# Optimization experiments

Hardware: AMD Instinct MI355X
Metric: run time of the kernel (lower is better)

Reference implementation:

```python
import jax, jax.numpy as jnp
import numpy as np

N_NODES = 20000
N_EDGES = 320000
IN_FEATS = 256
H_FEATS = 256


def setup_inputs() -> dict:
    key = jax.random.key(0)
    ks = jax.random.split(key, 8)
    s = 1.0 / np.sqrt(IN_FEATS)
    return {
        "features": jax.random.normal(ks[0], (N_NODES, IN_FEATS), jnp.float32),
        "src": jax.random.randint(ks[1], (N_EDGES,), 0, N_NODES, jnp.int32),
        "dst": jax.random.randint(ks[2], (N_EDGES,), 0, N_NODES, jnp.int32),
        "W_self1": jax.random.normal(ks[3], (IN_FEATS, H_FEATS), jnp.float32) * s,
        "W_neigh1": jax.random.normal(ks[4], (IN_FEATS, H_FEATS), jnp.float32) * s,
        "b1": jnp.zeros((H_FEATS,), jnp.float32),
        "W_self2": jax.random.normal(ks[5], (H_FEATS, H_FEATS), jnp.float32) * s,
        "W_neigh2": jax.random.normal(ks[6], (H_FEATS, H_FEATS), jnp.float32) * s,
        "b2": jnp.zeros((H_FEATS,), jnp.float32),
    }


def _sage_conv(h, src, dst, W_self, W_neigh, b, n_nodes):
    # mean aggregation of src features onto dst nodes (DGL SAGEConv 'mean')
    msg_sum = jax.ops.segment_sum(h[src], dst, num_segments=n_nodes)  # [N, d]
    deg = jax.ops.segment_sum(jnp.ones_like(dst, dtype=h.dtype), dst,
                              num_segments=n_nodes)  # [N]
    h_neigh = msg_sum / jnp.maximum(deg, 1.0)[:, None]  # isolated nodes -> 0
    return h @ W_self + h_neigh @ W_neigh + b


def reference(features, src, dst, W_self1, W_neigh1, b1, W_self2, W_neigh2, b2):
    n = features.shape[0]
    h = _sage_conv(features, src, dst, W_self1, W_neigh1, b1, n)
    h = jax.nn.relu(h)
    h = _sage_conv(h, src, dst, W_self2, W_neigh2, b2, n)
    # DotPredictor: per-edge dot product of src/dst embeddings
    score = jnp.sum(h[src] * h[dst], axis=1)  # [E]
    return score
```

## Files before the change

kernel.cpp:

```cpp
#include <hip/hip_runtime.h>
#include <hip/hip_bf16.h>
#include <stdint.h>

typedef __bf16 bf16_t;
typedef __bf16 bf16x8 __attribute__((ext_vector_type(8)));
typedef __bf16 bf16x4 __attribute__((ext_vector_type(4)));
typedef float f32x4 __attribute__((ext_vector_type(4)));

#define NFEAT 256
#define KDIM  512
#define BM 64
#define BN 128
#define BK 64

__device__ __forceinline__ void gload_lds16(const void* g, void* l) {
  __builtin_amdgcn_global_load_lds(
      (const __attribute__((address_space(1))) unsigned int*)g,
      (__attribute__((address_space(3))) unsigned int*)l, 16, 0, 0);
}

__device__ int g_b1, g_b2, g_b3, g_done;
__device__ int g_part[128];

__device__ __forceinline__ void grid_bar(int* ctr, int nb) {
  __syncthreads();
  if (threadIdx.x == 0) {
    __threadfence();
    atomicAdd(ctr, 1);
    while (atomicAdd(ctr, 0) < nb) { }
  }
  __syncthreads();
}

__global__ __launch_bounds__(256) void k_graph(
    const int* __restrict__ src, const int* __restrict__ dst,
    int* __restrict__ deg, int* __restrict__ offsets, int* __restrict__ cursor,
    float* __restrict__ inv_deg, int* __restrict__ csr_src, int2* __restrict__ epack,
    int nE, int n, int nb) {
  const int b   = blockIdx.x;
  const int tid = threadIdx.x;
  const int gt  = b * 256 + tid;
  const int G   = nb * 256;

  for (int e = gt; e < nE; e += G) atomicAdd(&deg[dst[e]], 1);
  grid_bar(&g_b1, nb);

  __shared__ int s[256], p[256];
  const int i = b * 256 + tid;
  const int d = (i < n) ? atomicAdd(&deg[i], 0) : 0;
  s[tid] = d;
  __syncthreads();
  for (int off = 1; off < 256; off <<= 1) {
    int v = (tid >= off) ? s[tid - off] : 0;
    __syncthreads();
    s[tid] += v;
    __syncthreads();
  }
  if (tid == 255) atomicExch(&g_part[b], s[255]);
  grid_bar(&g_b2, nb);

  int pv = 0;
  if (tid < b) pv = atomicAdd(&g_part[tid], 0);
  p[tid] = pv;
  __syncthreads();
  for (int off = 128; off; off >>= 1) {
    if (tid < off) p[tid] += p[tid + off];
    __syncthreads();
  }
  const int block_excl = p[0];
  if (i < n) {
    int excl = block_excl + s[tid] - d;
    offsets[i] = excl;
    atomicExch(&cursor[i], excl);
    inv_deg[i] = 1.0f / (float)(d > 1 ? d : 1);
  }
  grid_bar(&g_b3, nb);

  for (int e = gt; e < nE; e += G) {
    int dd = dst[e];
    int ss = src[e];
    int pos = atomicAdd(&cursor[dd], 1);
    csr_src[pos] = ss;
    epack[pos] = make_int2((dd << 16) | ss, e);
  }

  __syncthreads();
  if (tid == 0) {
    int old = atomicAdd(&g_done, 1);
    if (old == nb - 1) {
      atomicExch(&g_b1, 0);
      atomicExch(&g_b2, 0);
      atomicExch(&g_b3, 0);
      atomicExch(&g_done, 0);
    }
  }
}

__global__ void k_prep(const float* __restrict__ F,
                       const float* __restrict__ Ws1, const float* __restrict__ Wn1,
                       const float* __restrict__ Ws2, const float* __restrict__ Wn2,
                       bf16_t* __restrict__ WT1, bf16_t* __restrict__ WT2,
                       bf16_t* __restrict__ X,
                       int* __restrict__ deg, int nNodes, int mpad) {
  int t = blockIdx.x * blockDim.x + threadIdx.x;
  if (t < mpad) deg[t] = 0;
  if (t < 2 * NFEAT * KDIM) {
    int layer = t >> 17;
    int r = t & (NFEAT * KDIM - 1);
    int n = r >> 9;
    int k = r & 511;
    const float* Ws = layer ? Ws2 : Ws1;
    const float* Wn = layer ? Wn2 : Wn1;
    float v = (k < NFEAT) ? Ws[k * NFEAT + n] : Wn[(k - NFEAT) * NFEAT + n];
    (layer ? WT2 : WT1)[r] = (bf16_t)v;
  }
  int n = t >> 6;
  int c = (t & 63) * 4;
  if (n < mpad) {
    float4 v = make_float4(0.f, 0.f, 0.f, 0.f);
    if (n < nNodes) v = *(const float4*)&F[(size_t)n * NFEAT + c];
    bf16x4 o;
    o[0] = (bf16_t)v.x; o[1] = (bf16_t)v.y; o[2] = (bf16_t)v.z; o[3] = (bf16_t)v.w;
    *(bf16x4*)&X[(size_t)n * KDIM + c] = o;
  }
}

__global__ __launch_bounds__(256) void k_agg(const bf16_t* __restrict__ Hin,
                                             bf16_t* __restrict__ Hout,
                                             const int* __restrict__ csr_src,
                                             const int* __restrict__ offsets,
                                             const int* __restrict__ deg,
                                             const float* __restrict__ inv_deg,
                                             int instride, int outstride) {
  const int n   = blockIdx.x * 8 + (threadIdx.x >> 5);
  const int l32 = threadIdx.x & 31;
  const int beg = offsets[n];
  const int cnt = deg[n];
  const size_t colo = (size_t)l32 * 8;

  float acc[8] = {0.f, 0.f, 0.f, 0.f, 0.f, 0.f, 0.f, 0.f};

  int s[4];
  #pragma unroll
  for (int q = 0; q < 4; ++q) s[q] = (q < cnt) ? csr_src[beg + q] : -1;

  for (int i = 0; i < cnt; i += 4) {
    bf16x8 v[4];
    bool h[4];
    #pragma unroll
    for (int q = 0; q < 4; ++q) {
      h[q] = (s[q] >= 0);
      if (h[q]) v[q] = *(const bf16x8*)&Hin[(size_t)s[q] * instride + colo];
    }
    #pragma unroll
    for (int q = 0; q < 4; ++q) {
      int j = i + 4 + q;
      s[q] = (j < cnt) ? csr_src[beg + j] : -1;
    }
    #pragma unroll
    for (int q = 0; q < 4; ++q) {
      if (h[q]) {
        #pragma unroll
        for (int e = 0; e < 8; ++e) acc[e] += (float)v[q][e];
      }
    }
  }

  float w = inv_deg[n];
  bf16x8 o;
  #pragma unroll
  for (int e = 0; e < 8; ++e) o[e] = (bf16_t)(acc[e] * w);
  *(bf16x8*)&Hout[(size_t)n * outstride + NFEAT + colo] = o;
}

__global__ __launch_bounds__(256, 3) void k_gemm(const bf16_t* __restrict__ A,
                                                 const bf16_t* __restrict__ BT,
                                                 const float* __restrict__ bias,
                                                 bf16_t* __restrict__ Cout,
                                                 int ostride, int relu) {
  __shared__ __align__(16) bf16_t As[2][BM * BK];
  __shared__ __align__(16) bf16_t Bs[2][BN * BK];
  const int tid  = threadIdx.x;
  const int lane = tid & 63;
  const int wave = tid >> 6;
  const int wr = wave >> 1, wc = wave & 1;
  const int m0 = blockIdx.x * BM;
  const int n0 = blockIdx.y * BN;
  const int l15 = lane & 15;
  const int lk8 = (lane >> 4) * 8;

  f32x4 acc[2][4] = {};

  auto stage = [&](int buf, int kt) {
    const int k0 = kt * BK;
    #pragma unroll
    for (int i = 0; i < 2; ++i) {
      int idx = i * 256 + tid;
      int row = idx >> 3;
      int c8  = (idx & 7) * 8;
      gload_lds16(A + (size_t)(m0 + row) * KDIM + k0 + c8,
                  (char*)&As[buf][0] + (i * 256 + wave * 64) * 16);
    }
    #pragma unroll
    for (int i = 0; i < 4; ++i) {
      int idx = i * 256 + tid;
      int row = idx >> 3;
      int c8  = (idx & 7) * 8;
      gload_lds16(BT + (size_t)(n0 + row) * KDIM + k0 + c8,
                  (char*)&Bs[buf][0] + (i * 256 + wave * 64) * 16);
    }
  };

  auto compute = [&](int buf) {
    #pragma unroll
    for (int kk = 0; kk < 2; ++kk) {
      bf16x8 af[2], bfr[4];
      #pragma unroll
      for (int m = 0; m < 2; ++m) {
        int row = wr * 32 + m * 16 + l15;
        af[m] = *(const bf16x8*)&As[buf][row * BK + kk * 32 + lk8];
      }
      #pragma unroll
      for (int n = 0; n < 4; ++n) {
        int col = wc * 64 + n * 16 + l15;
        bfr[n] = *(const bf16x8*)&Bs[buf][col * BK + kk * 32 + lk8];
      }
      #pragma unroll
      for (int m = 0; m < 2; ++m)
        #pragma unroll
        for (int n = 0; n < 4; ++n)
          acc[m][n] = __builtin_amdgcn_mfma_f32_16x16x32_bf16(af[m], bfr[n], acc[m][n], 0, 0, 0);
    }
  };

  stage(0, 0);
  __syncthreads();
  const int nt = KDIM / BK;
  int cur = 0;
  for (int t = 0; t < nt; ++t) {
    if (t + 1 < nt) stage(cur ^ 1, t + 1);
    compute(cur);
    __syncthreads();
    cur ^= 1;
  }

  #pragma unroll
  for (int n = 0; n < 4; ++n) {
    int col = n0 + wc * 64 + n * 16 + l15;
    float bv = bias[col];
    #pragma unroll
    for (int m = 0; m < 2; ++m) {
      int rbase = m0 + wr * 32 + m * 16 + (lane >> 4) * 4;
      #pragma unroll
      for (int j = 0; j < 4; ++j) {
        float v = acc[m][n][j] + bv;
        if (relu) v = fmaxf(v, 0.f);
        Cout[(size_t)(rbase + j) * ostride + col] = (bf16_t)v;
      }
    }
  }
}

__global__ __launch_bounds__(256) void k_edge_dot(const bf16_t* __restrict__ H,
                                                  const int2* __restrict__ epack,
                                                  float* __restrict__ out, int nE) {
  const int wid  = (blockIdx.x * blockDim.x + threadIdx.x) >> 6;
  const int lane = threadIdx.x & 63;
  const int l15  = lane & 15;
  const int hi   = lane >> 4;
  const int e0   = wid * 16;
  if (e0 >= nE) return;
  int pos = e0 + l15;
  if (pos >= nE) pos = nE - 1;

  const int2 e = epack[pos];
  const int s = e.x & 0xFFFF;
  const int d = ((unsigned)e.x) >> 16;
  const bf16_t* ps = H + (size_t)s * NFEAT + hi * 8;
  const bf16_t* pd = H + (size_t)d * NFEAT + hi * 8;

  f32x4 acc = {0.f, 0.f, 0.f, 0.f};
  #pragma unroll
  for (int ks = 0; ks < 8; ++ks) {
    bf16x8 a = *(const bf16x8*)(ps + ks * 32);
    bf16x8 b = *(const bf16x8*)(pd + ks * 32);
    acc = __builtin_amdgcn_mfma_f32_16x16x32_bf16(a, b, acc, 0, 0, 0);
  }

  if ((l15 >> 2) == hi && (e0 + l15) < nE) {
    int j = l15 & 3;
    float v = acc[0];
    v = (j == 1) ? acc[1] : v;
    v = (j == 2) ? acc[2] : v;
    v = (j == 3) ? acc[3] : v;
    out[e.y] = v;
  }
}


extern "C" void kernel_launch(void* const* d_in, const int* in_sizes, int n_in,
                              void* d_out, int out_size, void* d_ws, size_t ws_size,
                              hipStream_t stream) {
  const float* features = (const float*)d_in[0];
  const int*   src      = (const int*)d_in[1];
  const int*   dst      = (const int*)d_in[2];
  const float* Wself1   = (const float*)d_in[3];
  const float* Wneigh1  = (const float*)d_in[4];
  const float* b1       = (const float*)d_in[5];
  const float* Wself2   = (const float*)d_in[6];
  const float* Wneigh2  = (const float*)d_in[7];
  const float* b2       = (const float*)d_in[8];
  float* score = (float*)d_out;

  const int nNodes = in_sizes[0] / NFEAT;
  const int nE     = in_sizes[1];
  const int mpad   = ((nNodes + 127) / 128) * 128;

  char* ws = (char*)d_ws;
  size_t off = 0;
  auto alloc = [&](size_t bytes) { char* p = ws + off; off += (bytes + 255) & ~(size_t)255; return p; };
  bf16_t* Xcat1   = (bf16_t*)alloc((size_t)mpad * KDIM * 2);
  bf16_t* Xcat2   = (bf16_t*)alloc((size_t)mpad * KDIM * 2);
  bf16_t* H2      = (bf16_t*)alloc((size_t)mpad * NFEAT * 2);
  bf16_t* WT1     = (bf16_t*)alloc((size_t)NFEAT * KDIM * 2);
  bf16_t* WT2     = (bf16_t*)alloc((size_t)NFEAT * KDIM * 2);
  int*    deg     = (int*)alloc((size_t)mpad * 4);
  int*    offsets = (int*)alloc((size_t)mpad * 4);
  int*    cursor  = (int*)alloc((size_t)mpad * 4);
  float*  inv_deg = (float*)alloc((size_t)mpad * 4);
  int*    csr_src = (int*)alloc((size_t)nE * 4);
  int2*   epack   = (int2*)alloc((size_t)nE * 8);

  const int nb = (mpad + 255) / 256;

  k_prep<<<(mpad * 64 + 255) / 256, 256, 0, stream>>>(features, Wself1, Wneigh1,
                                                      Wself2, Wneigh2, WT1, WT2,
                                                      Xcat1, deg, nNodes, mpad);

  k_graph<<<nb, 256, 0, stream>>>(src, dst, deg, offsets, cursor, inv_deg,
                                  csr_src, epack, nE, mpad, nb);

  k_agg<<<mpad / 8, 256, 0, stream>>>(Xcat1, Xcat1, csr_src, offsets, deg, inv_deg, KDIM, KDIM);
  dim3 ggrid(mpad / BM, NFEAT / BN);
  k_gemm<<<ggrid, 256, 0, stream>>>(Xcat1, WT1, b1, Xcat2, KDIM, 1);

  k_agg<<<mpad / 8, 256, 0, stream>>>(Xcat2, Xcat2, csr_src, offsets, deg, inv_deg, KDIM, KDIM);
  k_gemm<<<ggrid, 256, 0, stream>>>(Xcat2, WT2, b2, H2, NFEAT, 0);

  const int nWaves = (nE + 15) / 16;
  k_edge_dot<<<(nWaves + 3) / 4, 256, 0, stream>>>(H2, epack, score, nE);
}
```

Baseline: 165.8 us.

## Fuse prep into persistent graph-build kernel with fixed grid and sleeping barriers

Merges the feature/weight conversion and degree zeroing kernel into the CSR-build kernel, which now runs as a persistent grid of fixed size using grid-stride loops and an extra grid barrier. The scan phases are restricted to the first blocks while all blocks share the atomic-heavy edge phases, spreading edge work over more blocks. The barrier spin now sleeps between polls. This saves one launch and should raise parallelism for the edge loops, but relies on all 640 blocks being co-resident and adds a fourth grid-wide barrier.

```diff
diff --git a/kernel.cpp b/kernel.cpp
--- a/kernel.cpp
+++ b/kernel.cpp
@@ -12,6 +12,7 @@
 #define BM 64
 #define BN 128
 #define BK 64
+#define NBB 640
 
 __device__ __forceinline__ void gload_lds16(const void* g, void* l) {
   __builtin_amdgcn_global_load_lds(
@@ -19,92 +20,37 @@
       (__attribute__((address_space(3))) unsigned int*)l, 16, 0, 0);
 }
 
-__device__ int g_b1, g_b2, g_b3, g_done;
+__device__ int g_bar[4];
+__device__ int g_done;
 __device__ int g_part[128];
 
-__device__ __forceinline__ void grid_bar(int* ctr, int nb) {
+__device__ __forceinline__ void grid_bar(int idx, int nbB) {
+  __threadfence();
   __syncthreads();
   if (threadIdx.x == 0) {
-    __threadfence();
-    atomicAdd(ctr, 1);
-    while (atomicAdd(ctr, 0) < nb) { }
+    atomicAdd(&g_bar[idx], 1);
+    while (atomicAdd(&g_bar[idx], 0) < nbB) __builtin_amdgcn_s_sleep(2);
   }
   __syncthreads();
 }
 
 __global__ __launch_bounds__(256) void k_graph(
+    const float* __restrict__ F,
+    const float* __restrict__ Ws1, const float* __restrict__ Wn1,
+    const float* __restrict__ Ws2, const float* __restrict__ Wn2,
+    bf16_t* __restrict__ WT1, bf16_t* __restrict__ WT2,
+    bf16_t* __restrict__ X,
     const int* __restrict__ src, const int* __restrict__ dst,
     int* __restrict__ deg, int* __restrict__ offsets, int* __restrict__ cursor,
     float* __restrict__ inv_deg, int* __restrict__ csr_src, int2* __restrict__ epack,
-    int nE, int n, int nb) {
+    int nNodes, int mpad, int nE, int nbS) {
   const int b   = blockIdx.x;
   const int tid = threadIdx.x;
   const int gt  = b * 256 + tid;
-  const int G   = nb * 256;
-
-  for (int e = gt; e < nE; e += G) atomicAdd(&deg[dst[e]], 1);
-  grid_bar(&g_b1, nb);
-
-  __shared__ int s[256], p[256];
-  const int i = b * 256 + tid;
-  const int d = (i < n) ? atomicAdd(&deg[i], 0) : 0;
-  s[tid] = d;
-  __syncthreads();
-  for (int off = 1; off < 256; off <<= 1) {
-    int v = (tid >= off) ? s[tid - off] : 0;
-    __syncthreads();
-    s[tid] += v;
-    __syncthreads();
-  }
-  if (tid == 255) atomicExch(&g_part[b], s[255]);
-  grid_bar(&g_b2, nb);
-
-  int pv = 0;
-  if (tid < b) pv = atomicAdd(&g_part[tid], 0);
-  p[tid] = pv;
-  __syncthreads();
-  for (int off = 128; off; off >>= 1) {
-    if (tid < off) p[tid] += p[tid + off];
-    __syncthreads();
-  }
-  const int block_excl = p[0];
-  if (i < n) {
-    int excl = block_excl + s[tid] - d;
-    offsets[i] = excl;
-    atomicExch(&cursor[i], excl);
-    inv_deg[i] = 1.0f / (float)(d > 1 ? d : 1);
-  }
-  grid_bar(&g_b3, nb);
-
-  for (int e = gt; e < nE; e += G) {
-    int dd = dst[e];
-    int ss = src[e];
-    int pos = atomicAdd(&cursor[dd], 1);
-    csr_src[pos] = ss;
-    epack[pos] = make_int2((dd << 16) | ss, e);
-  }
-
-  __syncthreads();
-  if (tid == 0) {
-    int old = atomicAdd(&g_done, 1);
-    if (old == nb - 1) {
-      atomicExch(&g_b1, 0);
-      atomicExch(&g_b2, 0);
-      atomicExch(&g_b3, 0);
-      atomicExch(&g_done, 0);
-    }
-  }
-}
-
-__global__ void k_prep(const float* __restrict__ F,
-                       const float* __restrict__ Ws1, const float* __restrict__ Wn1,
-                       const float* __restrict__ Ws2, const float* __restrict__ Wn2,
-                       bf16_t* __restrict__ WT1, bf16_t* __restrict__ WT2,
-                       bf16_t* __restrict__ X,
-                       int* __restrict__ deg, int nNodes, int mpad) {
-  int t = blockIdx.x * blockDim.x + threadIdx.x;
-  if (t < mpad) deg[t] = 0;
-  if (t < 2 * NFEAT * KDIM) {
+  const int G   = NBB * 256;
+
+  for (int t = gt; t < mpad; t += G) atomicExch(&deg[t], 0);
+  for (int t = gt; t < 2 * NFEAT * KDIM; t += G) {
     int layer = t >> 17;
     int r = t & (NFEAT * KDIM - 1);
     int n = r >> 9;
@@ -114,14 +60,74 @@
     float v = (k < NFEAT) ? Ws[k * NFEAT + n] : Wn[(k - NFEAT) * NFEAT + n];
     (layer ? WT2 : WT1)[r] = (bf16_t)v;
   }
-  int n = t >> 6;
-  int c = (t & 63) * 4;
-  if (n < mpad) {
+  for (int t = gt; t < mpad * 64; t += G) {
+    int n = t >> 6;
+    int c = (t & 63) * 4;
     float4 v = make_float4(0.f, 0.f, 0.f, 0.f);
     if (n < nNodes) v = *(const float4*)&F[(size_t)n * NFEAT + c];
     bf16x4 o;
     o[0] = (bf16_t)v.x; o[1] = (bf16_t)v.y; o[2] = (bf16_t)v.z; o[3] = (bf16_t)v.w;
     *(bf16x4*)&X[(size_t)n * KDIM + c] = o;
+  }
+  grid_bar(0, NBB);
+
+  for (int e = gt; e < nE; e += G) atomicAdd(&deg[dst[e]], 1);
+  grid_bar(1, NBB);
+
+  __shared__ int s[256], p[256];
+  int d = 0;
+  if (b < nbS) {
+    const int i = b * 256 + tid;
+    d = (i < mpad) ? atomicAdd(&deg[i], 0) : 0;
+    s[tid] = d;
+    __syncthreads();
+    for (int off = 1; off < 256; off <<= 1) {
+      int v = (tid >= off) ? s[tid - off] : 0;
+      __syncthreads();
+      s[tid] += v;
+      __syncthreads();
+    }
+    if (tid == 255) atomicExch(&g_part[b], s[255]);
+  }
+  grid_bar(2, NBB);
+
+  if (b < nbS) {
+    int pv = 0;
+    if (tid < b) pv = atomicAdd(&g_part[tid], 0);
+    p[tid] = pv;
+    __syncthreads();
+    for (int off = 128; off; off >>= 1) {
+      if (tid < off) p[tid] += p[tid + off];
+      __syncthreads();
+    }
+    const int i = b * 256 + tid;
+    if (i < mpad) {
+      int excl = p[0] + s[tid] - d;
+      offsets[i] = excl;
+      atomicExch(&cursor[i], excl);
+      inv_deg[i] = 1.0f / (float)(d > 1 ? d : 1);
+    }
+  }
+  grid_bar(3, NBB);
+
+  for (int e = gt; e < nE; e += G) {
+    int dd = dst[e];
+    int ss = src[e];
+    int pos = atomicAdd(&cursor[dd], 1);
+    csr_src[pos] = ss;
+    epack[pos] = make_int2((dd << 16) | ss, e);
+  }
+
+  __syncthreads();
+  if (tid == 0) {
+    int old = atomicAdd(&g_done, 1);
+    if (old == NBB - 1) {
+      atomicExch(&g_bar[0], 0);
+      atomicExch(&g_bar[1], 0);
+      atomicExch(&g_bar[2], 0);
+      atomicExch(&g_bar[3], 0);
+      atomicExch(&g_done, 0);
+    }
   }
 }
 
@@ -331,14 +337,12 @@
   int*    csr_src = (int*)alloc((size_t)nE * 4);
   int2*   epack   = (int2*)alloc((size_t)nE * 8);
 
-  const int nb = (mpad + 255) / 256;
-
-  k_prep<<<(mpad * 64 + 255) / 256, 256, 0, stream>>>(features, Wself1, Wneigh1,
-                                                      Wself2, Wneigh2, WT1, WT2,
-                                                      Xcat1, deg, nNodes, mpad);
-
-  k_graph<<<nb, 256, 0, stream>>>(src, dst, deg, offsets, cursor, inv_deg,
-                                  csr_src, epack, nE, mpad, nb);
+  const int nbS = (mpad + 255) / 256;
+
+  k_graph<<<NBB, 256, 0, stream>>>(features, Wself1, Wneigh1, Wself2, Wneigh2,
+                                   WT1, WT2, Xcat1, src, dst,
+                                   deg, offsets, cursor, inv_deg, csr_src, epack,
+                                   nNodes, mpad, nE, nbS);
 
   k_agg<<<mpad / 8, 256, 0, stream>>>(Xcat1, Xcat1, csr_src, offsets, deg, inv_deg, KDIM, KDIM);
   dim3 ggrid(mpad / BM, NFEAT / BN);
```

After: 436.8 us. 163% more time.
